# Performance work log

Measured on AMD Instinct MI355X. Metric: run time of the kernel, lower is better.

The kernel has to match this reference:

```python
import jax, jax.numpy as jnp
import numpy as np

B, T, F, H = 512, 512, 32, 64  # batch, lag, n_features, hidden_sizes[0]


def _lstm_layer(x_seq, Wih, Whh, bih, bhh):
    """Single LSTM layer, batch_first input [B,T,Fin] -> [B,T,H].
    PyTorch gate order: i, f, g, o."""
    # Precompute input projections for all timesteps (one big GEMM)
    xg = jnp.einsum('btf,gf->btg', x_seq, Wih) + bih + bhh  # [B,T,4H]
    xg_t = jnp.transpose(xg, (1, 0, 2))  # [T,B,4H]
    h0 = jnp.zeros((x_seq.shape[0], Whh.shape[1]), x_seq.dtype)
    c0 = jnp.zeros_like(h0)

    def step(carry, g_t):
        h, c = carry
        gates = g_t + h @ Whh.T  # [B,4H]
        i, f, g, o = jnp.split(gates, 4, axis=-1)
        i = jax.nn.sigmoid(i)
        f = jax.nn.sigmoid(f)
        g = jnp.tanh(g)
        o = jax.nn.sigmoid(o)
        c = f * c + i * g
        h = o * jnp.tanh(c)
        return (h, c), h

    (_, _), hs = jax.lax.scan(step, (h0, c0), xg_t)  # hs: [T,B,H]
    return jnp.transpose(hs, (1, 0, 2))  # [B,T,H]


def setup_inputs() -> dict:
    key = jax.random.key(0)
    ks = jax.random.split(key, 12)
    s_in = 1.0 / np.sqrt(H)
    u = lambda k, shape: jax.random.uniform(k, shape, jnp.float32, -s_in, s_in)
    return {
        'x': jax.random.normal(ks[0], (B, T, F), jnp.float32),
        'Wih0': u(ks[1], (4 * H, F)),
        'Whh0': u(ks[2], (4 * H, H)),
        'bih0': u(ks[3], (4 * H,)),
        'bhh0': u(ks[4], (4 * H,)),
        'Wih1': u(ks[5], (4 * H, H)),
        'Whh1': u(ks[6], (4 * H, H)),
        'bih1': u(ks[7], (4 * H,)),
        'bhh1': u(ks[8], (4 * H,)),
        'fcW': u(ks[9], (1, H)),
        'fcb': u(ks[10], (1,)),
    }


def reference(x, Wih0, Whh0, bih0, bhh0, Wih1, Whh1, bih1, bhh1, fcW, fcb):
    h1 = _lstm_layer(x, Wih0, Whh0, bih0, bhh0)   # [B,T,H]
    h2 = _lstm_layer(h1, Wih1, Whh1, bih1, bhh1)  # [B,T,H]  (dropout=0 at inference)
    last = h2[:, -1, :]                           # [B,H]
    out = last @ fcW.T + fcb                      # [B,1]
    return out.squeeze(-1)                        # [B]
```

## Files before the change

kernel.cpp:

```cpp
#include <hip/hip_runtime.h>
#include <math.h>

#define Bsz 512
#define Tsz 512
#define Fin 32
#define Hd 64
#define CHUNK 32
#define NCH (Tsz / CHUNK)

typedef float v2f __attribute__((ext_vector_type(2)));

__device__ __forceinline__ float fsig(float x) {
    return __builtin_amdgcn_rcpf(1.0f + __expf(-x));
}
__device__ __forceinline__ float ftanh(float x) {
    return fmaf(2.0f, __builtin_amdgcn_rcpf(1.0f + __expf(-2.0f * x)), -1.0f);
}

#define PIN4(v4) \
    asm volatile("" : "+v"((v4).x), "+v"((v4).y), "+v"((v4).z), "+v"((v4).w))

__global__ __launch_bounds__(256, 2)
void lstm_layer0(const float* __restrict__ x,
                 const float4* __restrict__ Wih4,
                 const float4* __restrict__ Whh4,
                 const float* __restrict__ bih,
                 const float* __restrict__ bhh,
                 float* __restrict__ h1out)
{
    __shared__ __align__(16) float xbuf[2][CHUNK * Fin];
    __shared__ __align__(16) float hcopy[4][Hd];
    __shared__ float glds[2][Hd * 5];

    const int tid  = threadIdx.x;
    const int lane = tid & 63;
    const int wv   = tid >> 6;
    const int wvu  = __builtin_amdgcn_readfirstlane(wv);
    const int b    = blockIdx.x;

    float4 wih[8];
#pragma unroll
    for (int q = 0; q < 8; ++q) wih[q] = Wih4[tid * 8 + q];
    float4 whh[16];
#pragma unroll
    for (int q = 0; q < 16; ++q) whh[q] = Whh4[tid * 16 + q];
    float bias = bih[tid] + bhh[tid];

    float c = 0.0f;
    hcopy[wv][lane] = 0.0f;

    const float4* xsrc = (const float4*)(x + (size_t)b * Tsz * Fin);
    ((float4*)xbuf[0])[tid] = xsrc[tid];
    float* hout = h1out + (size_t)b * Tsz * Hd + lane;
    __syncthreads();

    for (int ci = 0; ci < NCH; ++ci) {
        const int cur = ci & 1;
        if (ci + 1 < NCH)
            ((float4*)xbuf[cur ^ 1])[tid] = xsrc[(ci + 1) * (CHUNK * Fin / 4) + tid];
#pragma unroll
        for (int q = 0; q < 8; ++q)  PIN4(wih[q]);
#pragma unroll
        for (int q = 0; q < 16; ++q) PIN4(whh[q]);
#pragma unroll 1
        for (int ct = 0; ct < CHUNK; ct += 2) {
#pragma unroll
            for (int pp = 0; pp < 2; ++pp) {
                const float4* xrow = (const float4*)&xbuf[cur][(ct + pp) * Fin];
                const float4* hrow = (const float4*)&hcopy[wv][0];

                v2f a0 = {bias, 0.0f};
                v2f a1 = {0.0f, 0.0f};
#pragma unroll
                for (int q = 0; q < 8; ++q) {
                    float4 xv = xrow[q];
                    v2f b0 = {xv.x, xv.y}, b1 = {xv.z, xv.w};
                    v2f w0 = {wih[q].x, wih[q].y}, w1 = {wih[q].z, wih[q].w};
                    a0 = __builtin_elementwise_fma(b0, w0, a0);
                    a1 = __builtin_elementwise_fma(b1, w1, a1);
                }
#pragma unroll
                for (int q = 0; q < 16; ++q) {
                    float4 hv = hrow[q];
                    v2f b0 = {hv.x, hv.y}, b1 = {hv.z, hv.w};
                    v2f w0 = {whh[q].x, whh[q].y}, w1 = {whh[q].z, whh[q].w};
                    a0 = __builtin_elementwise_fma(b0, w0, a0);
                    a1 = __builtin_elementwise_fma(b1, w1, a1);
                }
                float a = (a0.x + a0.y) + (a1.x + a1.y);
                if (wvu == 2) glds[pp][lane * 5 + wv] = ftanh(a);
                else          glds[pp][lane * 5 + wv] = fsig(a);
                __syncthreads();
                float gi = glds[pp][lane * 5 + 0];
                float gf = glds[pp][lane * 5 + 1];
                float gg = glds[pp][lane * 5 + 2];
                float go = glds[pp][lane * 5 + 3];
                c = fmaf(gf, c, gi * gg);
                float h = go * ftanh(c);
                hcopy[wv][lane] = h;
                if (wvu == 0)
                    hout[(size_t)(ci * CHUNK + ct + pp) * Hd] = h;
            }
        }
    }
}

__global__ __launch_bounds__(256, 2)
void lstm_layer1_fc(const float* __restrict__ h1,
                    const float4* __restrict__ Wih4,
                    const float4* __restrict__ Whh4,
                    const float* __restrict__ bih,
                    const float* __restrict__ bhh,
                    const float* __restrict__ fcW,
                    const float* __restrict__ fcb,
                    float* __restrict__ out)
{
    __shared__ __align__(16) float xbuf[2][CHUNK * Hd];
    __shared__ __align__(16) float hcopy[4][Hd];
    __shared__ float glds[2][Hd * 5];

    const int tid  = threadIdx.x;
    const int lane = tid & 63;
    const int wv   = tid >> 6;
    const int wvu  = __builtin_amdgcn_readfirstlane(wv);
    const int b    = blockIdx.x;

    float4 wih[16];
#pragma unroll
    for (int q = 0; q < 16; ++q) wih[q] = Wih4[tid * 16 + q];
    float4 whh[16];
#pragma unroll
    for (int q = 0; q < 16; ++q) whh[q] = Whh4[tid * 16 + q];
    float bias = bih[tid] + bhh[tid];

    float c  = 0.0f;
    float hl = 0.0f;
    hcopy[wv][lane] = 0.0f;

    const float4* xsrc = (const float4*)(h1 + (size_t)b * Tsz * Hd);
    ((float4*)xbuf[0])[tid]       = xsrc[tid];
    ((float4*)xbuf[0])[tid + 256] = xsrc[tid + 256];
    __syncthreads();

    for (int ci = 0; ci < NCH; ++ci) {
        const int cur = ci & 1;
        if (ci + 1 < NCH) {
            ((float4*)xbuf[cur ^ 1])[tid]       = xsrc[(ci + 1) * (CHUNK * Hd / 4) + tid];
            ((float4*)xbuf[cur ^ 1])[tid + 256] = xsrc[(ci + 1) * (CHUNK * Hd / 4) + tid + 256];
        }
#pragma unroll
        for (int q = 0; q < 16; ++q) PIN4(wih[q]);
#pragma unroll
        for (int q = 0; q < 16; ++q) PIN4(whh[q]);
#pragma unroll 1
        for (int ct = 0; ct < CHUNK; ct += 2) {
#pragma unroll
            for (int pp = 0; pp < 2; ++pp) {
                const float4* xrow = (const float4*)&xbuf[cur][(ct + pp) * Hd];
                const float4* hrow = (const float4*)&hcopy[wv][0];

                v2f a0 = {bias, 0.0f};
                v2f a1 = {0.0f, 0.0f};
#pragma unroll
                for (int q = 0; q < 16; ++q) {
                    float4 xv = xrow[q];
                    v2f b0 = {xv.x, xv.y}, b1 = {xv.z, xv.w};
                    v2f w0 = {wih[q].x, wih[q].y}, w1 = {wih[q].z, wih[q].w};
                    a0 = __builtin_elementwise_fma(b0, w0, a0);
                    a1 = __builtin_elementwise_fma(b1, w1, a1);
                }
#pragma unroll
                for (int q = 0; q < 16; ++q) {
                    float4 hv = hrow[q];
                    v2f b0 = {hv.x, hv.y}, b1 = {hv.z, hv.w};
                    v2f w0 = {whh[q].x, whh[q].y}, w1 = {whh[q].z, whh[q].w};
                    a0 = __builtin_elementwise_fma(b0, w0, a0);
                    a1 = __builtin_elementwise_fma(b1, w1, a1);
                }
                float a = (a0.x + a0.y) + (a1.x + a1.y);
                if (wvu == 2) glds[pp][lane * 5 + wv] = ftanh(a);
                else          glds[pp][lane * 5 + wv] = fsig(a);
                __syncthreads();
                float gi = glds[pp][lane * 5 + 0];
                float gf = glds[pp][lane * 5 + 1];
                float gg = glds[pp][lane * 5 + 2];
                float go = glds[pp][lane * 5 + 3];
                c  = fmaf(gf, c, gi * gg);
                hl = go * ftanh(c);
                hcopy[wv][lane] = hl;
            }
        }
    }
    if (wvu == 0) {
        float psum = hl * fcW[lane];
#pragma unroll
        for (int off = 32; off > 0; off >>= 1)
            psum += __shfl_down(psum, off);
        if (lane == 0) out[b] = psum + fcb[0];
    }
}

extern "C" void kernel_launch(void* const* d_in, const int* in_sizes, int n_in,
                              void* d_out, int out_size, void* d_ws, size_t ws_size,
                              hipStream_t stream)
{
    const float* x    = (const float*)d_in[0];
    const float* Wih0 = (const float*)d_in[1];
    const float* Whh0 = (const float*)d_in[2];
    const float* bih0 = (const float*)d_in[3];
    const float* bhh0 = (const float*)d_in[4];
    const float* Wih1 = (const float*)d_in[5];
    const float* Whh1 = (const float*)d_in[6];
    const float* bih1 = (const float*)d_in[7];
    const float* bhh1 = (const float*)d_in[8];
    const float* fcW  = (const float*)d_in[9];
    const float* fcb  = (const float*)d_in[10];
    float* out = (float*)d_out;
    float* h1  = (float*)d_ws;

    lstm_layer0<<<dim3(Bsz), dim3(256), 0, stream>>>(
        x, (const float4*)Wih0, (const float4*)Whh0, bih0, bhh0, h1);
    lstm_layer1_fc<<<dim3(Bsz), dim3(256), 0, stream>>>(
        h1, (const float4*)Wih1, (const float4*)Whh1, bih1, bhh1, fcW, fcb, out);
}
```

Before: 746.1 us.

## Prefetch x rows into registers and compute next-step input projection before barrier

Replaces the LDS double-buffered x chunk with per-thread register prefetch of the next timestep's input row straight from global memory (uniform address, broadcast). The input projection for step t+1 is computed in the shadow of the barrier after gate activations, so the barrier-critical path only holds the recurrent h·Whh dot product. This removes LDS reads of x, but adds 8 or 16 extra float4 registers per thread, which risks occupancy or spills, and issues a global load every step whose latency must be hidden within one step.

Measured after the change: 864.9 us. 1.16x slower.

```diff
diff --git a/kernel.cpp b/kernel.cpp
--- a/kernel.cpp
+++ b/kernel.cpp
@@ -28,7 +28,6 @@
                  const float* __restrict__ bhh,
                  float* __restrict__ h1out)
 {
-    __shared__ __align__(16) float xbuf[2][CHUNK * Fin];
     __shared__ __align__(16) float hcopy[4][Hd];
     __shared__ float glds[2][Hd * 5];
 
@@ -44,20 +43,35 @@
     float4 whh[16];
 #pragma unroll
     for (int q = 0; q < 16; ++q) whh[q] = Whh4[tid * 16 + q];
-    float bias = bih[tid] + bhh[tid];
+    const float bias = bih[tid] + bhh[tid];
 
     float c = 0.0f;
     hcopy[wv][lane] = 0.0f;
 
     const float4* xsrc = (const float4*)(x + (size_t)b * Tsz * Fin);
-    ((float4*)xbuf[0])[tid] = xsrc[tid];
     float* hout = h1out + (size_t)b * Tsz * Hd + lane;
+
+    float4 xv[8];
+#pragma unroll
+    for (int q = 0; q < 8; ++q) xv[q] = xsrc[q];
+    float ax;
+    {
+        v2f a0 = {bias, 0.0f}, a1 = {0.0f, 0.0f};
+#pragma unroll
+        for (int q = 0; q < 8; ++q) {
+            float4 t4 = xv[q];
+            v2f b0 = {t4.x, t4.y}, b1 = {t4.z, t4.w};
+            v2f w0 = {wih[q].x, wih[q].y}, w1 = {wih[q].z, wih[q].w};
+            a0 = __builtin_elementwise_fma(b0, w0, a0);
+            a1 = __builtin_elementwise_fma(b1, w1, a1);
+        }
+        ax = (a0.x + a0.y) + (a1.x + a1.y);
+    }
+#pragma unroll
+    for (int q = 0; q < 8; ++q) xv[q] = xsrc[8 + q];
     __syncthreads();
 
     for (int ci = 0; ci < NCH; ++ci) {
-        const int cur = ci & 1;
-        if (ci + 1 < NCH)
-            ((float4*)xbuf[cur ^ 1])[tid] = xsrc[(ci + 1) * (CHUNK * Fin / 4) + tid];
 #pragma unroll
         for (int q = 0; q < 8; ++q)  PIN4(wih[q]);
 #pragma unroll
@@ -66,19 +80,10 @@
         for (int ct = 0; ct < CHUNK; ct += 2) {
 #pragma unroll
             for (int pp = 0; pp < 2; ++pp) {
-                const float4* xrow = (const float4*)&xbuf[cur][(ct + pp) * Fin];
+                const int t = ci * CHUNK + ct + pp;
                 const float4* hrow = (const float4*)&hcopy[wv][0];
 
-                v2f a0 = {bias, 0.0f};
-                v2f a1 = {0.0f, 0.0f};
-#pragma unroll
-                for (int q = 0; q < 8; ++q) {
-                    float4 xv = xrow[q];
-                    v2f b0 = {xv.x, xv.y}, b1 = {xv.z, xv.w};
-                    v2f w0 = {wih[q].x, wih[q].y}, w1 = {wih[q].z, wih[q].w};
-                    a0 = __builtin_elementwise_fma(b0, w0, a0);
-                    a1 = __builtin_elementwise_fma(b1, w1, a1);
-                }
+                v2f a0 = {ax, 0.0f}, a1 = {0.0f, 0.0f};
 #pragma unroll
                 for (int q = 0; q < 16; ++q) {
                     float4 hv = hrow[q];
@@ -90,6 +95,23 @@
                 float a = (a0.x + a0.y) + (a1.x + a1.y);
                 if (wvu == 2) glds[pp][lane * 5 + wv] = ftanh(a);
                 else          glds[pp][lane * 5 + wv] = fsig(a);
+
+                {
+                    v2f a0x = {bias, 0.0f}, a1x = {0.0f, 0.0f};
+#pragma unroll
+                    for (int q = 0; q < 8; ++q) {
+                        float4 t4 = xv[q];
+                        v2f b0 = {t4.x, t4.y}, b1 = {t4.z, t4.w};
+                        v2f w0 = {wih[q].x, wih[q].y}, w1 = {wih[q].z, wih[q].w};
+                        a0x = __builtin_elementwise_fma(b0, w0, a0x);
+                        a1x = __builtin_elementwise_fma(b1, w1, a1x);
+                    }
+                    ax = (a0x.x + a0x.y) + (a1x.x + a1x.y);
+                }
+                const int tn = (t + 2 < Tsz) ? (t + 2) : (Tsz - 1);
+#pragma unroll
+                for (int q = 0; q < 8; ++q) xv[q] = xsrc[(size_t)tn * 8 + q];
+
                 __syncthreads();
                 float gi = glds[pp][lane * 5 + 0];
                 float gf = glds[pp][lane * 5 + 1];
@@ -98,8 +120,7 @@
                 c = fmaf(gf, c, gi * gg);
                 float h = go * ftanh(c);
                 hcopy[wv][lane] = h;
-                if (wvu == 0)
-                    hout[(size_t)(ci * CHUNK + ct + pp) * Hd] = h;
+                if (wvu == 0) hout[(size_t)t * Hd] = h;
             }
         }
     }
@@ -115,7 +136,6 @@
                     const float* __restrict__ fcb,
                     float* __restrict__ out)
 {
-    __shared__ __align__(16) float xbuf[2][CHUNK * Hd];
     __shared__ __align__(16) float hcopy[4][Hd];
     __shared__ float glds[2][Hd * 5];
 
@@ -131,23 +151,35 @@
     float4 whh[16];
 #pragma unroll
     for (int q = 0; q < 16; ++q) whh[q] = Whh4[tid * 16 + q];
-    float bias = bih[tid] + bhh[tid];
+    const float bias = bih[tid] + bhh[tid];
 
     float c  = 0.0f;
     float hl = 0.0f;
     hcopy[wv][lane] = 0.0f;
 
     const float4* xsrc = (const float4*)(h1 + (size_t)b * Tsz * Hd);
-    ((float4*)xbuf[0])[tid]       = xsrc[tid];
-    ((float4*)xbuf[0])[tid + 256] = xsrc[tid + 256];
+
+    float4 xv[16];
+#pragma unroll
+    for (int q = 0; q < 16; ++q) xv[q] = xsrc[q];
+    float ax;
+    {
+        v2f a0 = {bias, 0.0f}, a1 = {0.0f, 0.0f};
+#pragma unroll
+        for (int q = 0; q < 16; ++q) {
+            float4 t4 = xv[q];
+            v2f b0 = {t4.x, t4.y}, b1 = {t4.z, t4.w};
+            v2f w0 = {wih[q].x, wih[q].y}, w1 = {wih[q].z, wih[q].w};
+            a0 = __builtin_elementwise_fma(b0, w0, a0);
+            a1 = __builtin_elementwise_fma(b1, w1, a1);
+        }
+        ax = (a0.x + a0.y) + (a1.x + a1.y);
+    }
+#pragma unroll
+    for (int q = 0; q < 16; ++q) xv[q] = xsrc[16 + q];
     __syncthreads();
 
     for (int ci = 0; ci < NCH; ++ci) {
-        const int cur = ci & 1;
-        if (ci + 1 < NCH) {
-            ((float4*)xbuf[cur ^ 1])[tid]       = xsrc[(ci + 1) * (CHUNK * Hd / 4) + tid];
-            ((float4*)xbuf[cur ^ 1])[tid + 256] = xsrc[(ci + 1) * (CHUNK * Hd / 4) + tid + 256];
-        }
 #pragma unroll
         for (int q = 0; q < 16; ++q) PIN4(wih[q]);
 #pragma unroll
@@ -156,19 +188,10 @@
         for (int ct = 0; ct < CHUNK; ct += 2) {
 #pragma unroll
             for (int pp = 0; pp < 2; ++pp) {
-                const float4* xrow = (const float4*)&xbuf[cur][(ct + pp) * Hd];
+                const int t = ci * CHUNK + ct + pp;
                 const float4* hrow = (const float4*)&hcopy[wv][0];
 
-                v2f a0 = {bias, 0.0f};
-                v2f a1 = {0.0f, 0.0f};
-#pragma unroll
-                for (int q = 0; q < 16; ++q) {
-                    float4 xv = xrow[q];
-                    v2f b0 = {xv.x, xv.y}, b1 = {xv.z, xv.w};
-                    v2f w0 = {wih[q].x, wih[q].y}, w1 = {wih[q].z, wih[q].w};
-                    a0 = __builtin_elementwise_fma(b0, w0, a0);
-                    a1 = __builtin_elementwise_fma(b1, w1, a1);
-                }
+                v2f a0 = {ax, 0.0f}, a1 = {0.0f, 0.0f};
 #pragma unroll
                 for (int q = 0; q < 16; ++q) {
                     float4 hv = hrow[q];
@@ -180,6 +203,23 @@
                 float a = (a0.x + a0.y) + (a1.x + a1.y);
                 if (wvu == 2) glds[pp][lane * 5 + wv] = ftanh(a);
                 else          glds[pp][lane * 5 + wv] = fsig(a);
+
+                {
+                    v2f a0x = {bias, 0.0f}, a1x = {0.0f, 0.0f};
+#pragma unroll
+                    for (int q = 0; q < 16; ++q) {
+                        float4 t4 = xv[q];
+                        v2f b0 = {t4.x, t4.y}, b1 = {t4.z, t4.w};
+                        v2f w0 = {wih[q].x, wih[q].y}, w1 = {wih[q].z, wih[q].w};
+                        a0x = __builtin_elementwise_fma(b0, w0, a0x);
+                        a1x = __builtin_elementwise_fma(b1, w1, a1x);
+                    }
+                    ax = (a0x.x + a0x.y) + (a1x.x + a1x.y);
+                }
+                const int tn = (t + 2 < Tsz) ? (t + 2) : (Tsz - 1);
+#pragma unroll
+                for (int q = 0; q < 16; ++q) xv[q] = xsrc[(size_t)tn * 16 + q];
+
                 __syncthreads();
                 float gi = glds[pp][lane * 5 + 0];
                 float gf = glds[pp][lane * 5 + 1];
```

## Process two batch rows per block to share register-resident weights

Applied to the files above, without the earlier changes.

Each block now runs the LSTM recurrence for two batch elements at once, reusing the register-held Wih/Whh weights for both sequences and halving the grid to 256 blocks. This amortizes the per-step barrier and weight loads across two independent recurrences and gives more independent FMAs to hide latency. In exchange, launch bounds drop to one block per SM, registers and LDS per block roughly double, and with 256 blocks on a large GPU occupancy and parallelism fall.

Measured after the change: 1.039 ms. 1.39x slower.

```diff
diff --git a/kernel.cpp b/kernel.cpp
--- a/kernel.cpp
+++ b/kernel.cpp
@@ -20,7 +20,7 @@
 #define PIN4(v4) \
     asm volatile("" : "+v"((v4).x), "+v"((v4).y), "+v"((v4).z), "+v"((v4).w))
 
-__global__ __launch_bounds__(256, 2)
+__global__ __launch_bounds__(256, 1)
 void lstm_layer0(const float* __restrict__ x,
                  const float4* __restrict__ Wih4,
                  const float4* __restrict__ Whh4,
@@ -28,15 +28,16 @@
                  const float* __restrict__ bhh,
                  float* __restrict__ h1out)
 {
-    __shared__ __align__(16) float xbuf[2][CHUNK * Fin];
-    __shared__ __align__(16) float hcopy[4][Hd];
-    __shared__ float glds[2][Hd * 5];
+    __shared__ __align__(16) float xbuf[2][2][CHUNK * Fin];
+    __shared__ __align__(16) float hcopy[2][4][Hd];
+    __shared__ float glds[2][2][Hd * 5];
 
     const int tid  = threadIdx.x;
     const int lane = tid & 63;
     const int wv   = tid >> 6;
     const int wvu  = __builtin_amdgcn_readfirstlane(wv);
-    const int b    = blockIdx.x;
+    const int b0   = blockIdx.x * 2;
+    const int b1   = b0 + 1;
 
     float4 wih[8];
 #pragma unroll
@@ -44,20 +45,26 @@
     float4 whh[16];
 #pragma unroll
     for (int q = 0; q < 16; ++q) whh[q] = Whh4[tid * 16 + q];
-    float bias = bih[tid] + bhh[tid];
-
-    float c = 0.0f;
-    hcopy[wv][lane] = 0.0f;
-
-    const float4* xsrc = (const float4*)(x + (size_t)b * Tsz * Fin);
-    ((float4*)xbuf[0])[tid] = xsrc[tid];
-    float* hout = h1out + (size_t)b * Tsz * Hd + lane;
+    const float bias = bih[tid] + bhh[tid];
+
+    float c0 = 0.0f, c1 = 0.0f;
+    hcopy[0][wv][lane] = 0.0f;
+    hcopy[1][wv][lane] = 0.0f;
+
+    const float4* xs0 = (const float4*)(x + (size_t)b0 * Tsz * Fin);
+    const float4* xs1 = (const float4*)(x + (size_t)b1 * Tsz * Fin);
+    ((float4*)xbuf[0][0])[tid] = xs0[tid];
+    ((float4*)xbuf[1][0])[tid] = xs1[tid];
+    float* hout0 = h1out + (size_t)b0 * Tsz * Hd + lane;
+    float* hout1 = h1out + (size_t)b1 * Tsz * Hd + lane;
     __syncthreads();
 
     for (int ci = 0; ci < NCH; ++ci) {
         const int cur = ci & 1;
-        if (ci + 1 < NCH)
-            ((float4*)xbuf[cur ^ 1])[tid] = xsrc[(ci + 1) * (CHUNK * Fin / 4) + tid];
+        if (ci + 1 < NCH) {
+            ((float4*)xbuf[0][cur ^ 1])[tid] = xs0[(ci + 1) * (CHUNK * Fin / 4) + tid];
+            ((float4*)xbuf[1][cur ^ 1])[tid] = xs1[(ci + 1) * (CHUNK * Fin / 4) + tid];
+        }
 #pragma unroll
         for (int q = 0; q < 8; ++q)  PIN4(wih[q]);
 #pragma unroll
@@ -66,46 +73,70 @@
         for (int ct = 0; ct < CHUNK; ct += 2) {
 #pragma unroll
             for (int pp = 0; pp < 2; ++pp) {
-                const float4* xrow = (const float4*)&xbuf[cur][(ct + pp) * Fin];
-                const float4* hrow = (const float4*)&hcopy[wv][0];
-
-                v2f a0 = {bias, 0.0f};
-                v2f a1 = {0.0f, 0.0f};
+                const int t = ci * CHUNK + ct + pp;
+                const float4* xr0 = (const float4*)&xbuf[0][cur][(ct + pp) * Fin];
+                const float4* xr1 = (const float4*)&xbuf[1][cur][(ct + pp) * Fin];
+                const float4* hr0 = (const float4*)&hcopy[0][wv][0];
+                const float4* hr1 = (const float4*)&hcopy[1][wv][0];
+
+                v2f p0 = {bias, 0.0f}, p1 = {0.0f, 0.0f};
+                v2f q0 = {bias, 0.0f}, q1 = {0.0f, 0.0f};
 #pragma unroll
                 for (int q = 0; q < 8; ++q) {
-                    float4 xv = xrow[q];
-                    v2f b0 = {xv.x, xv.y}, b1 = {xv.z, xv.w};
-                    v2f w0 = {wih[q].x, wih[q].y}, w1 = {wih[q].z, wih[q].w};
-                    a0 = __builtin_elementwise_fma(b0, w0, a0);
-                    a1 = __builtin_elementwise_fma(b1, w1, a1);
+                    float4 w4 = wih[q];
+                    v2f w0 = {w4.x, w4.y}, w1 = {w4.z, w4.w};
+                    float4 xa = xr0[q], xb = xr1[q];
+                    v2f a0 = {xa.x, xa.y}, a1 = {xa.z, xa.w};
+                    v2f b0v = {xb.x, xb.y}, b1v = {xb.z, xb.w};
+                    p0 = __builtin_elementwise_fma(a0, w0, p0);
+                    p1 = __builtin_elementwise_fma(a1, w1, p1);
+                    q0 = __builtin_elementwise_fma(b0v, w0, q0);
+                    q1 = __builtin_elementwise_fma(b1v, w1, q1);
                 }
 #pragma unroll
                 for (int q = 0; q < 16; ++q) {
-                    float4 hv = hrow[q];
-                    v2f b0 = {hv.x, hv.y}, b1 = {hv.z, hv.w};
-                    v2f w0 = {whh[q].x, whh[q].y}, w1 = {whh[q].z, whh[q].w};
-                    a0 = __builtin_elementwise_fma(b0, w0, a0);
-                    a1 = __builtin_elementwise_fma(b1, w1, a1);
-                }
-                float a = (a0.x + a0.y) + (a1.x + a1.y);
-                if (wvu == 2) glds[pp][lane * 5 + wv] = ftanh(a);
-                else          glds[pp][lane * 5 + wv] = fsig(a);
+                    float4 w4 = whh[q];
+                    v2f w0 = {w4.x, w4.y}, w1 = {w4.z, w4.w};
+                    float4 ha = hr0[q], hb = hr1[q];
+                    v2f a0 = {ha.x, ha.y}, a1 = {ha.z, ha.w};
+                    v2f b0v = {hb.x, hb.y}, b1v = {hb.z, hb.w};
+                    p0 = __builtin_elementwise_fma(a0, w0, p0);
+                    p1 = __builtin_elementwise_fma(a1, w1, p1);
+                    q0 = __builtin_elementwise_fma(b0v, w0, q0);
+                    q1 = __builtin_elementwise_fma(b1v, w1, q1);
+                }
+                float aa = (p0.x + p0.y) + (p1.x + p1.y);
+                float ab = (q0.x + q0.y) + (q1.x + q1.y);
+                if (wvu == 2) {
+                    glds[0][pp][lane * 5 + wv] = ftanh(aa);
+                    glds[1][pp][lane * 5 + wv] = ftanh(ab);
+                } else {
+                    glds[0][pp][lane * 5 + wv] = fsig(aa);
+                    glds[1][pp][lane * 5 + wv] = fsig(ab);
+                }
                 __syncthreads();
-                float gi = glds[pp][lane * 5 + 0];
-                float gf = glds[pp][lane * 5 + 1];
-                float gg = glds[pp][lane * 5 + 2];
-                float go = glds[pp][lane * 5 + 3];
-                c = fmaf(gf, c, gi * gg);
-                float h = go * ftanh(c);
-                hcopy[wv][lane] = h;
-                if (wvu == 0)
-                    hout[(size_t)(ci * CHUNK + ct + pp) * Hd] = h;
+                float gi0 = glds[0][pp][lane * 5 + 0];
+                float gf0 = glds[0][pp][lane * 5 + 1];
+                float gg0 = glds[0][pp][lane * 5 + 2];
+                float go0 = glds[0][pp][lane * 5 + 3];
+                float gi1 = glds[1][pp][lane * 5 + 0];
+                float gf1 = glds[1][pp][lane * 5 + 1];
+                float gg1 = glds[1][pp][lane * 5 + 2];
+                float go1 = glds[1][pp][lane * 5 + 3];
+                c0 = fmaf(gf0, c0, gi0 * gg0);
+                c1 = fmaf(gf1, c1, gi1 * gg1);
+                float h0 = go0 * ftanh(c0);
+                float h1 = go1 * ftanh(c1);
+                hcopy[0][wv][lane] = h0;
+                hcopy[1][wv][lane] = h1;
+                if (wvu == 0) hout0[(size_t)t * Hd] = h0;
+                if (wvu == 1) hout1[(size_t)t * Hd] = h1;
             }
         }
     }
 }
 
-__global__ __launch_bounds__(256, 2)
+__global__ __launch_bounds__(256, 1)
 void lstm_layer1_fc(const float* __restrict__ h1,
                     const float4* __restrict__ Wih4,
                     const float4* __restrict__ Whh4,
@@ -115,15 +146,16 @@
                     const float* __restrict__ fcb,
                     float* __restrict__ out)
 {
-    __shared__ __align__(16) float xbuf[2][CHUNK * Hd];
-    __shared__ __align__(16) float hcopy[4][Hd];
-    __shared__ float glds[2][Hd * 5];
+    __shared__ __align__(16) float xbuf[2][2][CHUNK * Hd];
+    __shared__ __align__(16) float hcopy[2][4][Hd];
+    __shared__ float glds[2][2][Hd * 5];
 
     const int tid  = threadIdx.x;
     const int lane = tid & 63;
     const int wv   = tid >> 6;
     const int wvu  = __builtin_amdgcn_readfirstlane(wv);
-    const int b    = blockIdx.x;
+    const int b0   = blockIdx.x * 2;
+    const int b1   = b0 + 1;
 
     float4 wih[16];
 #pragma unroll
@@ -131,22 +163,29 @@
     float4 whh[16];
 #pragma unroll
     for (int q = 0; q < 16; ++q) whh[q] = Whh4[tid * 16 + q];
-    float bias = bih[tid] + bhh[tid];
-
-    float c  = 0.0f;
-    float hl = 0.0f;
-    hcopy[wv][lane] = 0.0f;
-
-    const float4* xsrc = (const float4*)(h1 + (size_t)b * Tsz * Hd);
-    ((float4*)xbuf[0])[tid]       = xsrc[tid];
-    ((float4*)xbuf[0])[tid + 256] = xsrc[tid + 256];
+    const float bias = bih[tid] + bhh[tid];
+
+    float c0 = 0.0f, c1 = 0.0f;
+    float hl0 = 0.0f, hl1 = 0.0f;
+    hcopy[0][wv][lane] = 0.0f;
+    hcopy[1][wv][lane] = 0.0f;
+
+    const float4* xs0 = (const float4*)(h1 + (size_t)b0 * Tsz * Hd);
+    const float4* xs1 = (const float4*)(h1 + (size_t)b1 * Tsz * Hd);
+    ((float4*)xbuf[0][0])[tid]       = xs0[tid];
+    ((float4*)xbuf[0][0])[tid + 256] = xs0[tid + 256];
+    ((float4*)xbuf[1][0])[tid]       = xs1[tid];
+    ((float4*)xbuf[1][0])[tid + 256] = xs1[tid + 256];
     __syncthreads();
 
     for (int ci = 0; ci < NCH; ++ci) {
         const int cur = ci & 1;
         if (ci + 1 < NCH) {
-            ((float4*)xbuf[cur ^ 1])[tid]       = xsrc[(ci + 1) * (CHUNK * Hd / 4) + tid];
-            ((float4*)xbuf[cur ^ 1])[tid + 256] = xsrc[(ci + 1) * (CHUNK * Hd / 4) + tid + 256];
+            const int base = (ci + 1) * (CHUNK * Hd / 4);
+            ((float4*)xbuf[0][cur ^ 1])[tid]       = xs0[base + tid];
+            ((float4*)xbuf[0][cur ^ 1])[tid + 256] = xs0[base + tid + 256];
+            ((float4*)xbuf[1][cur ^ 1])[tid]       = xs1[base + tid];
+            ((float4*)xbuf[1][cur ^ 1])[tid + 256] = xs1[base + tid + 256];
         }
 #pragma unroll
         for (int q = 0; q < 16; ++q) PIN4(wih[q]);
@@ -156,47 +195,77 @@
         for (int ct = 0; ct < CHUNK; ct += 2) {
 #pragma unroll
             for (int pp = 0; pp < 2; ++pp) {
-                const float4* xrow = (const float4*)&xbuf[cur][(ct + pp) * Hd];
-                const float4* hrow = (const float4*)&hcopy[wv][0];
-
-                v2f a0 = {bias, 0.0f};
-                v2f a1 = {0.0f, 0.0f};
+                const float4* xr0 = (const float4*)&xbuf[0][cur][(ct + pp) * Hd];
+                const float4* xr1 = (const float4*)&xbuf[1][cur][(ct + pp) * Hd];
+                const float4* hr0 = (const float4*)&hcopy[0][wv][0];
+                const float4* hr1 = (const float4*)&hcopy[1][wv][0];
+
+                v2f p0 = {bias, 0.0f}, p1 = {0.0f, 0.0f};
+                v2f q0 = {bias, 0.0f}, q1 = {0.0f, 0.0f};
 #pragma unroll
                 for (int q = 0; q < 16; ++q) {
-                    float4 xv = xrow[q];
-                    v2f b0 = {xv.x, xv.y}, b1 = {xv.z, xv.w};
-                    v2f w0 = {wih[q].x, wih[q].y}, w1 = {wih[q].z, wih[q].w};
-                    a0 = __builtin_elementwise_fma(b0, w0, a0);
-                    a1 = __builtin_elementwise_fma(b1, w1, a1);
+                    float4 w4 = wih[q];
+                    v2f w0 = {w4.x, w4.y}, w1 = {w4.z, w4.w};
+                    float4 xa = xr0[q], xb = xr1[q];
+                    v2f a0 = {xa.x, xa.y}, a1 = {xa.z, xa.w};
+                    v2f b0v = {xb.x, xb.y}, b1v = {xb.z, xb.w};
+                    p0 = __builtin_elementwise_fma(a0, w0, p0);
+                    p1 = __builtin_elementwise_fma(a1, w1, p1);
+                    q0 = __builtin_elementwise_fma(b0v, w0, q0);
+                    q1 = __builtin_elementwise_fma(b1v, w1, q1);
                 }
 #pragma unroll
                 for (int q = 0; q < 16; ++q) {
-                    float4 hv = hrow[q];
-                    v2f b0 = {hv.x, hv.y}, b1 = {hv.z, hv.w};
-                    v2f w0 = {whh[q].x, whh[q].y}, w1 = {whh[q].z, whh[q].w};
-                    a0 = __builtin_elementwise_fma(b0, w0, a0);
-                    a1 = __builtin_elementwise_fma(b1, w1, a1);
-                }
-                float a = (a0.x + a0.y) + (a1.x + a1.y);
-                if (wvu == 2) glds[pp][lane * 5 + wv] = ftanh(a);
-                else          glds[pp][lane * 5 + wv] = fsig(a);
+                    float4 w4 = whh[q];
+                    v2f w0 = {w4.x, w4.y}, w1 = {w4.z, w4.w};
+                    float4 ha = hr0[q], hb = hr1[q];
+                    v2f a0 = {ha.x, ha.y}, a1 = {ha.z, ha.w};
+                    v2f b0v = {hb.x, hb.y}, b1v = {hb.z, hb.w};
+                    p0 = __builtin_elementwise_fma(a0, w0, p0);
+                    p1 = __builtin_elementwise_fma(a1, w1, p1);
+                    q0 = __builtin_elementwise_fma(b0v, w0, q0);
+                    q1 = __builtin_elementwise_fma(b1v, w1, q1);
+                }
+                float aa = (p0.x + p0.y) + (p1.x + p1.y);
+                float ab = (q0.x + q0.y) + (q1.x + q1.y);
+                if (wvu == 2) {
+                    glds[0][pp][lane * 5 + wv] = ftanh(aa);
+                    glds[1][pp][lane * 5 + wv] = ftanh(ab);
+                } else {
+                    glds[0][pp][lane * 5 + wv] = fsig(aa);
+                    glds[1][pp][lane * 5 + wv] = fsig(ab);
+                }
                 __syncthreads();
-                float gi = glds[pp][lane * 5 + 0];
-                float gf = glds[pp][lane * 5 + 1];
-                float gg = glds[pp][lane * 5 + 2];
-                float go = glds[pp][lane * 5 + 3];
-                c  = fmaf(gf, c, gi * gg);
-                hl = go * ftanh(c);
-                hcopy[wv][lane] = hl;
+                float gi0 = glds[0][pp][lane * 5 + 0];
+                float gf0 = glds[0][pp][lane * 5 + 1];
+                float gg0 = glds[0][pp][lane * 5 + 2];
+                float go0 = glds[0][pp][lane * 5 + 3];
+                float gi1 = glds[1][pp][lane * 5 + 0];
+                float gf1 = glds[1][pp][lane * 5 + 1];
+                float gg1 = glds[1][pp][lane * 5 + 2];
+                float go1 = glds[1][pp][lane * 5 + 3];
+                c0  = fmaf(gf0, c0, gi0 * gg0);
+                c1  = fmaf(gf1, c1, gi1 * gg1);
+                hl0 = go0 * ftanh(c0);
+                hl1 = go1 * ftanh(c1);
+                hcopy[0][wv][lane] = hl0;
+                hcopy[1][wv][lane] = hl1;
             }
         }
     }
     if (wvu == 0) {
-        float psum = hl * fcW[lane];
+        float psum = hl0 * fcW[lane];
 #pragma unroll
         for (int off = 32; off > 0; off >>= 1)
             psum += __shfl_down(psum, off);
-        if (lane == 0) out[b] = psum + fcb[0];
+        if (lane == 0) out[b0] = psum + fcb[0];
+    }
+    if (wvu == 1) {
+        float psum = hl1 * fcW[lane];
+#pragma unroll
+        for (int off = 32; off > 0; off >>= 1)
+            psum += __shfl_down(psum, off);
+        if (lane == 0) out[b1] = psum + fcb[0];
     }
 }
 
@@ -218,8 +287,8 @@
     float* out = (float*)d_out;
     float* h1  = (float*)d_ws;
 
-    lstm_layer0<<<dim3(Bsz), dim3(256), 0, stream>>>(
+    lstm_layer0<<<dim3(Bsz / 2), dim3(256), 0, stream>>>(
         x, (const float4*)Wih0, (const float4*)Whh0, bih0, bhh0, h1);
-    lstm_layer1_fc<<<dim3(Bsz), dim3(256), 0, stream>>>(
+    lstm_layer1_fc<<<dim3(Bsz / 2), dim3(256), 0, stream>>>(
         h1, (const float4*)Wih1, (const float4*)Whh1, bih1, bhh1, fcW, fcb, out);
 }
```

## Interleave gates across lanes with shuffle exchange and overlap next-step input projection

Applied to the files above, without the earlier changes.

Each thread now owns gate q of hidden unit d (tid = 4d+q), so the four gates of one unit sit in adjacent lanes and are exchanged with two xor shuffles instead of an LDS round trip plus barrier. The h vector is double-buffered in a single shared row. The input projection for step t+1 is computed after h is produced, off the recurrent critical path. A unified sigmoid-based tanh for the g gate removes the per-wave branch. One barrier per step remains. The cost is more shuffle traffic and a redundant final-h read from LDS for the FC.

Result: slower. 827.6 us (+10.9%).

```diff
diff --git a/kernel.cpp b/kernel.cpp
--- a/kernel.cpp
+++ b/kernel.cpp
@@ -29,78 +29,102 @@
                  float* __restrict__ h1out)
 {
     __shared__ __align__(16) float xbuf[2][CHUNK * Fin];
-    __shared__ __align__(16) float hcopy[4][Hd];
-    __shared__ float glds[2][Hd * 5];
-
-    const int tid  = threadIdx.x;
-    const int lane = tid & 63;
-    const int wv   = tid >> 6;
-    const int wvu  = __builtin_amdgcn_readfirstlane(wv);
-    const int b    = blockIdx.x;
+    __shared__ __align__(16) float hrow[2][Hd];
+
+    const int tid = threadIdx.x;
+    const int q   = tid & 3;
+    const int d   = tid >> 2;
+    const int b   = blockIdx.x;
+    const int r   = q * Hd + d;
 
     float4 wih[8];
 #pragma unroll
-    for (int q = 0; q < 8; ++q) wih[q] = Wih4[tid * 8 + q];
+    for (int k = 0; k < 8; ++k) wih[k] = Wih4[r * 8 + k];
     float4 whh[16];
 #pragma unroll
-    for (int q = 0; q < 16; ++q) whh[q] = Whh4[tid * 16 + q];
-    float bias = bih[tid] + bhh[tid];
+    for (int k = 0; k < 16; ++k) whh[k] = Whh4[r * 16 + k];
+    const float bias = bih[r] + bhh[r];
+    const float kq = (q == 2) ? 2.0f : 1.0f;
+    const float bq = (q == 2) ? -1.0f : 0.0f;
 
     float c = 0.0f;
-    hcopy[wv][lane] = 0.0f;
 
     const float4* xsrc = (const float4*)(x + (size_t)b * Tsz * Fin);
     ((float4*)xbuf[0])[tid] = xsrc[tid];
-    float* hout = h1out + (size_t)b * Tsz * Hd + lane;
+    if (tid < Hd) hrow[0][tid] = 0.0f;
+    float* hout = h1out + (size_t)b * Tsz * Hd;
     __syncthreads();
+
+    float ax;
+    {
+        const float4* xr = (const float4*)&xbuf[0][0];
+        v2f a0 = {bias, 0.0f}, a1 = {0.0f, 0.0f};
+#pragma unroll
+        for (int k = 0; k < 8; ++k) {
+            float4 xv = xr[k];
+            v2f b0 = {xv.x, xv.y}, b1 = {xv.z, xv.w};
+            v2f w0 = {wih[k].x, wih[k].y}, w1 = {wih[k].z, wih[k].w};
+            a0 = __builtin_elementwise_fma(b0, w0, a0);
+            a1 = __builtin_elementwise_fma(b1, w1, a1);
+        }
+        ax = (a0.x + a0.y) + (a1.x + a1.y);
+    }
 
     for (int ci = 0; ci < NCH; ++ci) {
         const int cur = ci & 1;
         if (ci + 1 < NCH)
             ((float4*)xbuf[cur ^ 1])[tid] = xsrc[(ci + 1) * (CHUNK * Fin / 4) + tid];
 #pragma unroll
-        for (int q = 0; q < 8; ++q)  PIN4(wih[q]);
-#pragma unroll
-        for (int q = 0; q < 16; ++q) PIN4(whh[q]);
+        for (int k = 0; k < 8; ++k)  PIN4(wih[k]);
+#pragma unroll
+        for (int k = 0; k < 16; ++k) PIN4(whh[k]);
 #pragma unroll 1
-        for (int ct = 0; ct < CHUNK; ct += 2) {
-#pragma unroll
-            for (int pp = 0; pp < 2; ++pp) {
-                const float4* xrow = (const float4*)&xbuf[cur][(ct + pp) * Fin];
-                const float4* hrow = (const float4*)&hcopy[wv][0];
-
-                v2f a0 = {bias, 0.0f};
-                v2f a1 = {0.0f, 0.0f};
-#pragma unroll
-                for (int q = 0; q < 8; ++q) {
-                    float4 xv = xrow[q];
+        for (int ct = 0; ct < CHUNK; ++ct) {
+            const int t = ci * CHUNK + ct;
+            const float4* hp = (const float4*)&hrow[t & 1][0];
+            v2f a0 = {ax, 0.0f}, a1 = {0.0f, 0.0f};
+#pragma unroll
+            for (int k = 0; k < 16; ++k) {
+                float4 hv = hp[k];
+                v2f b0 = {hv.x, hv.y}, b1 = {hv.z, hv.w};
+                v2f w0 = {whh[k].x, whh[k].y}, w1 = {whh[k].z, whh[k].w};
+                a0 = __builtin_elementwise_fma(b0, w0, a0);
+                a1 = __builtin_elementwise_fma(b1, w1, a1);
+            }
+            float a = (a0.x + a0.y) + (a1.x + a1.y);
+            float s   = fsig(kq * a);
+            float act = fmaf(kq, s, bq);
+            float x1 = __shfl_xor(act, 1);
+            float la = (q & 1) ? x1 : act;
+            float lb = (q & 1) ? act : x1;
+            float ra = __shfl_xor(la, 2);
+            float rb = __shfl_xor(lb, 2);
+            float gi = (q & 2) ? ra : la;
+            float gf = (q & 2) ? rb : lb;
+            float gg = (q & 2) ? la : ra;
+            float go = (q & 2) ? lb : rb;
+            c = fmaf(gf, c, gi * gg);
+            float h = go * ftanh(c);
+            if (q == 0) {
+                hrow[(t + 1) & 1][d] = h;
+                hout[(size_t)t * Hd + d] = h;
+            }
+            {
+                const float* xbase = (ct == CHUNK - 1) ? &xbuf[cur ^ 1][0]
+                                                       : &xbuf[cur][(ct + 1) * Fin];
+                const float4* xr = (const float4*)xbase;
+                v2f a0x = {bias, 0.0f}, a1x = {0.0f, 0.0f};
+#pragma unroll
+                for (int k = 0; k < 8; ++k) {
+                    float4 xv = xr[k];
                     v2f b0 = {xv.x, xv.y}, b1 = {xv.z, xv.w};
-                    v2f w0 = {wih[q].x, wih[q].y}, w1 = {wih[q].z, wih[q].w};
-                    a0 = __builtin_elementwise_fma(b0, w0, a0);
-                    a1 = __builtin_elementwise_fma(b1, w1, a1);
+                    v2f w0 = {wih[k].x, wih[k].y}, w1 = {wih[k].z, wih[k].w};
+                    a0x = __builtin_elementwise_fma(b0, w0, a0x);
+                    a1x = __builtin_elementwise_fma(b1, w1, a1x);
                 }
-#pragma unroll
-                for (int q = 0; q < 16; ++q) {
-                    float4 hv = hrow[q];
-                    v2f b0 = {hv.x, hv.y}, b1 = {hv.z, hv.w};
-                    v2f w0 = {whh[q].x, whh[q].y}, w1 = {whh[q].z, whh[q].w};
-                    a0 = __builtin_elementwise_fma(b0, w0, a0);
-                    a1 = __builtin_elementwise_fma(b1, w1, a1);
-                }
-                float a = (a0.x + a0.y) + (a1.x + a1.y);
-                if (wvu == 2) glds[pp][lane * 5 + wv] = ftanh(a);
-                else          glds[pp][lane * 5 + wv] = fsig(a);
-                __syncthreads();
-                float gi = glds[pp][lane * 5 + 0];
-                float gf = glds[pp][lane * 5 + 1];
-                float gg = glds[pp][lane * 5 + 2];
-                float go = glds[pp][lane * 5 + 3];
-                c = fmaf(gf, c, gi * gg);
-                float h = go * ftanh(c);
-                hcopy[wv][lane] = h;
-                if (wvu == 0)
-                    hout[(size_t)(ci * CHUNK + ct + pp) * Hd] = h;
-            }
+                ax = (a0x.x + a0x.y) + (a1x.x + a1x.y);
+            }
+            __syncthreads();
         }
     }
 }
@@ -116,87 +140,110 @@
                     float* __restrict__ out)
 {
     __shared__ __align__(16) float xbuf[2][CHUNK * Hd];
-    __shared__ __align__(16) float hcopy[4][Hd];
-    __shared__ float glds[2][Hd * 5];
-
-    const int tid  = threadIdx.x;
-    const int lane = tid & 63;
-    const int wv   = tid >> 6;
-    const int wvu  = __builtin_amdgcn_readfirstlane(wv);
-    const int b    = blockIdx.x;
+    __shared__ __align__(16) float hrow[2][Hd];
+
+    const int tid = threadIdx.x;
+    const int q   = tid & 3;
+    const int d   = tid >> 2;
+    const int b   = blockIdx.x;
+    const int r   = q * Hd + d;
 
     float4 wih[16];
 #pragma unroll
-    for (int q = 0; q < 16; ++q) wih[q] = Wih4[tid * 16 + q];
+    for (int k = 0; k < 16; ++k) wih[k] = Wih4[r * 16 + k];
     float4 whh[16];
 #pragma unroll
-    for (int q = 0; q < 16; ++q) whh[q] = Whh4[tid * 16 + q];
-    float bias = bih[tid] + bhh[tid];
-
-    float c  = 0.0f;
-    float hl = 0.0f;
-    hcopy[wv][lane] = 0.0f;
+    for (int k = 0; k < 16; ++k) whh[k] = Whh4[r * 16 + k];
+    const float bias = bih[r] + bhh[r];
+    const float kq = (q == 2) ? 2.0f : 1.0f;
+    const float bq = (q == 2) ? -1.0f : 0.0f;
+
+    float c = 0.0f;
 
     const float4* xsrc = (const float4*)(h1 + (size_t)b * Tsz * Hd);
     ((float4*)xbuf[0])[tid]       = xsrc[tid];
     ((float4*)xbuf[0])[tid + 256] = xsrc[tid + 256];
+    if (tid < Hd) hrow[0][tid] = 0.0f;
     __syncthreads();
+
+    float ax;
+    {
+        const float4* xr = (const float4*)&xbuf[0][0];
+        v2f a0 = {bias, 0.0f}, a1 = {0.0f, 0.0f};
+#pragma unroll
+        for (int k = 0; k < 16; ++k) {
+            float4 xv = xr[k];
+            v2f b0 = {xv.x, xv.y}, b1 = {xv.z, xv.w};
+            v2f w0 = {wih[k].x, wih[k].y}, w1 = {wih[k].z, wih[k].w};
+            a0 = __builtin_elementwise_fma(b0, w0, a0);
+            a1 = __builtin_elementwise_fma(b1, w1, a1);
+        }
+        ax = (a0.x + a0.y) + (a1.x + a1.y);
+    }
 
     for (int ci = 0; ci < NCH; ++ci) {
         const int cur = ci & 1;
         if (ci + 1 < NCH) {
-            ((float4*)xbuf[cur ^ 1])[tid]       = xsrc[(ci + 1) * (CHUNK * Hd / 4) + tid];
-            ((float4*)xbuf[cur ^ 1])[tid + 256] = xsrc[(ci + 1) * (CHUNK * Hd / 4) + tid + 256];
-        }
-#pragma unroll
-        for (int q = 0; q < 16; ++q) PIN4(wih[q]);
-#pragma unroll
-        for (int q = 0; q < 16; ++q) PIN4(whh[q]);
+            const int base = (ci + 1) * (CHUNK * Hd / 4);
+            ((float4*)xbuf[cur ^ 1])[tid]       = xsrc[base + tid];
+            ((float4*)xbuf[cur ^ 1])[tid + 256] = xsrc[base + tid + 256];
+        }
+#pragma unroll
+        for (int k = 0; k < 16; ++k) PIN4(wih[k]);
+#pragma unroll
+        for (int k = 0; k < 16; ++k) PIN4(whh[k]);
 #pragma unroll 1
-        for (int ct = 0; ct < CHUNK; ct += 2) {
-#pragma unroll
-            for (int pp = 0; pp < 2; ++pp) {
-                const float4* xrow = (const float4*)&xbuf[cur][(ct + pp) * Hd];
-                const float4* hrow = (const float4*)&hcopy[wv][0];
-
-                v2f a0 = {bias, 0.0f};
-                v2f a1 = {0.0f, 0.0f};
-#pragma unroll
-                for (int q = 0; q < 16; ++q) {
-                    float4 xv = xrow[q];
+        for (int ct = 0; ct < CHUNK; ++ct) {
+            const int t = ci * CHUNK + ct;
+            const float4* hp = (const float4*)&hrow[t & 1][0];
+            v2f a0 = {ax, 0.0f}, a1 = {0.0f, 0.0f};
+#pragma unroll
+            for (int k = 0; k < 16; ++k) {
+                float4 hv = hp[k];
+                v2f b0 = {hv.x, hv.y}, b1 = {hv.z, hv.w};
+                v2f w0 = {whh[k].x, whh[k].y}, w1 = {whh[k].z, whh[k].w};
+                a0 = __builtin_elementwise_fma(b0, w0, a0);
+                a1 = __builtin_elementwise_fma(b1, w1, a1);
+            }
+            float a = (a0.x + a0.y) + (a1.x + a1.y);
+            float s   = fsig(kq * a);
+            float act = fmaf(kq, s, bq);
+            float x1 = __shfl_xor(act, 1);
+            float la = (q & 1) ? x1 : act;
+            float lb = (q & 1) ? act : x1;
+            float ra = __shfl_xor(la, 2);
+            float rb = __shfl_xor(lb, 2);
+            float gi = (q & 2) ? ra : la;
+            float gf = (q & 2) ? rb : lb;
+            float gg = (q & 2) ? la : ra;
+            float go = (q & 2) ? lb : rb;
+            c = fmaf(gf, c, gi * gg);
+            float h = go * ftanh(c);
+            if (q == 0) hrow[(t + 1) & 1][d] = h;
+            {
+                const float* xbase = (ct == CHUNK - 1) ? &xbuf[cur ^ 1][0]
+                                                       : &xbuf[cur][(ct + 1) * Hd];
+                const float4* xr = (const float4*)xbase;
+                v2f a0x = {bias, 0.0f}, a1x = {0.0f, 0.0f};
+#pragma unroll
+                for (int k = 0; k < 16; ++k) {
+                    float4 xv = xr[k];
                     v2f b0 = {xv.x, xv.y}, b1 = {xv.z, xv.w};
-                    v2f w0 = {wih[q].x, wih[q].y}, w1 = {wih[q].z, wih[q].w};
-                    a0 = __builtin_elementwise_fma(b0, w0, a0);
-                    a1 = __builtin_elementwise_fma(b1, w1, a1);
+                    v2f w0 = {wih[k].x, wih[k].y}, w1 = {wih[k].z, wih[k].w};
+                    a0x = __builtin_elementwise_fma(b0, w0, a0x);
+                    a1x = __builtin_elementwise_fma(b1, w1, a1x);
                 }
-#pragma unroll
-                for (int q = 0; q < 16; ++q) {
-                    float4 hv = hrow[q];
-                    v2f b0 = {hv.x, hv.y}, b1 = {hv.z, hv.w};
-                    v2f w0 = {whh[q].x, whh[q].y}, w1 = {whh[q].z, whh[q].w};
-                    a0 = __builtin_elementwise_fma(b0, w0, a0);
-                    a1 = __builtin_elementwise_fma(b1, w1, a1);
-                }
-                float a = (a0.x + a0.y) + (a1.x + a1.y);
-                if (wvu == 2) glds[pp][lane * 5 + wv] = ftanh(a);
-                else          glds[pp][lane * 5 + wv] = fsig(a);
-                __syncthreads();
-                float gi = glds[pp][lane * 5 + 0];
-                float gf = glds[pp][lane * 5 + 1];
-                float gg = glds[pp][lane * 5 + 2];
-                float go = glds[pp][lane * 5 + 3];
-                c  = fmaf(gf, c, gi * gg);
-                hl = go * ftanh(c);
-                hcopy[wv][lane] = hl;
-            }
-        }
-    }
-    if (wvu == 0) {
-        float psum = hl * fcW[lane];
+                ax = (a0x.x + a0x.y) + (a1x.x + a1x.y);
+            }
+            __syncthreads();
+        }
+    }
+    if (tid < 64) {
+        float psum = hrow[0][tid] * fcW[tid];
 #pragma unroll
         for (int off = 32; off > 0; off >>= 1)
             psum += __shfl_down(psum, off);
-        if (lane == 0) out[b] = psum + fcb[0];
+        if (tid == 0) out[b] = psum + fcb[0];
     }
 }
 
```
